# Kernel optimization log

Measured on AMD Instinct MI355X. Metric: run time of the kernel, lower is better.

The kernel has to match this reference:

```python
import jax, jax.numpy as jnp
import numpy as np

BATCH = 32768
INPUT_DIM = 256
N_NEURONS = 128
MAX_DEGREE = 7  # D; features per input dim = D+1 = 8


def _cheb_features(x, degree):
    """Chebyshev T_0..T_degree of x [B, In] -> [B, In, degree+1] via recurrence.

    Matches torch.special.chebyshev_polynomial_t(x, n=d) for d = 0..degree.
    """
    T = [jnp.ones_like(x), x]
    for _ in range(2, degree + 1):
        T.append(2.0 * x * T[-1] - T[-2])
    return jnp.stack(T[: degree + 1], axis=-1)


def setup_inputs() -> dict:
    key = jax.random.key(0)
    k1, k2 = jax.random.split(key)
    # inputs in [0,1) keep Chebyshev values bounded, as in a normalized pipeline
    x = jax.random.uniform(k1, (BATCH, INPUT_DIM), dtype=jnp.float32)
    # per-neuron coefficient vectors over the dim-major [In*(D+1)] feature layout
    coeffs = jax.random.normal(k2, (N_NEURONS, INPUT_DIM * (MAX_DEGREE + 1)), dtype=jnp.float32) * 0.02
    return {"x": x, "coeffs": coeffs}


def reference(x, coeffs):
    B, In = x.shape
    D = coeffs.shape[1] // In - 1
    # [B, In, D+1] -> dim-major flatten matches torch.cat over per-dim stacks
    X = _cheb_features(x, D).reshape(B, In * (D + 1))
    # per-neuron dot products, then sum over neurons (KANLayer stack().sum(0))
    per_neuron = jnp.einsum("bf,nf->bn", X, coeffs)  # [B, n_neurons]
    return per_neuron.sum(axis=1, keepdims=True)  # [B, 1]
```

## Files before the change

### kernel.cpp

```cpp
#include <hip/hip_runtime.h>

#define BATCH     32768
#define IN_DIM    256
#define N_NEURONS 128
#define DEG1      8
#define FEAT      (IN_DIM * DEG1)
#define F4        (FEAT / 4)
#define XR4       (IN_DIM / 4)
#define RPW       16


__global__ __launch_bounds__(256) void reduce_coeffs(const float* __restrict__ coeffs,
                                                     float* __restrict__ csum) {
    __shared__ float4 part[256];
    const int t = threadIdx.x;
    const int c = t & 7;
    const int g = t >> 3;
    const int col4 = blockIdx.x * 8 + c;

    const float4* p = (const float4*)coeffs + (size_t)(g * 4) * F4 + col4;
    float4 s = make_float4(0.f, 0.f, 0.f, 0.f);
#pragma unroll
    for (int n = 0; n < 4; ++n) {
        float4 v = p[(size_t)n * F4];
        s.x += v.x; s.y += v.y; s.z += v.z; s.w += v.w;
    }
    part[t] = s;
    __syncthreads();
#pragma unroll
    for (int stride = 128; stride >= 8; stride >>= 1) {
        if (t < stride) {
            float4 o = part[t + stride];
            float4 m = part[t];
            m.x += o.x; m.y += o.y; m.z += o.z; m.w += o.w;
            part[t] = m;
        }
        __syncthreads();
    }
    if (t < 8) ((float4*)csum)[blockIdx.x * 8 + t] = part[t];
}

__global__ __launch_bounds__(256) void kan_fwd(const float* __restrict__ x,
                                               const float* __restrict__ csum,
                                               float* __restrict__ out) {
    const int lane = threadIdx.x & 63;
    const int wave = threadIdx.x >> 6;
    const int row0 = (blockIdx.x * 4 + wave) * RPW;

    float c[4][8];
    const float4* c4 = (const float4*)csum + (size_t)lane * 8;
#pragma unroll
    for (int j = 0; j < 4; ++j) {
        float4 a = c4[j * 2];
        float4 b = c4[j * 2 + 1];
        c[j][0] = a.x; c[j][1] = a.y; c[j][2] = a.z; c[j][3] = a.w;
        c[j][4] = b.x; c[j][5] = b.y; c[j][6] = b.z; c[j][7] = b.w;
    }

    float acc[RPW];
    const float4* xr = (const float4*)x + (size_t)row0 * XR4 + lane;
#pragma unroll
    for (int r = 0; r < RPW; ++r) {
        float4 xv = xr[(size_t)r * XR4];
        float xs[4] = {xv.x, xv.y, xv.z, xv.w};
        float a = 0.f;
#pragma unroll
        for (int j = 0; j < 4; ++j) {
            const float xx = xs[j];
            const float two_x = xx + xx;
            a = fmaf(c[j][1], xx, a + c[j][0]);
            float tp = 1.f, tc = xx;
#pragma unroll
            for (int d = 2; d < 8; ++d) {
                float tn = fmaf(two_x, tc, -tp);
                a = fmaf(c[j][d], tn, a);
                tp = tc; tc = tn;
            }
        }
        acc[r] = a;
    }

#pragma unroll
    for (int rq = 0; rq < RPW / 4; ++rq) {
        float s[4];
#pragma unroll
        for (int k = 0; k < 4; ++k) {
            float a = acc[rq * 4 + k];
#pragma unroll
            for (int off = 32; off > 0; off >>= 1) a += __shfl_down(a, off, 64);
            s[k] = a;
        }
        if (lane == 0)
            ((float4*)out)[row0 / 4 + rq] = make_float4(s[0], s[1], s[2], s[3]);
    }
}

extern "C" void kernel_launch(void* const* d_in, const int* in_sizes, int n_in,
                              void* d_out, int out_size, void* d_ws, size_t ws_size,
                              hipStream_t stream) {
    const float* x      = (const float*)d_in[0];
    const float* coeffs = (const float*)d_in[1];
    float* out  = (float*)d_out;
    float* csum = (float*)d_ws;

    reduce_coeffs<<<64, 256, 0, stream>>>(coeffs, csum);
    kan_fwd<<<BATCH / (4 * RPW), 256, 0, stream>>>(x, csum, out);
}
```

Before: 77.71 us.

## Fuse coefficient reduction into main kernel with per-block shared-memory csum

Merges the coefficient-sum kernel into the forward kernel so that each of 256 large blocks reduces all 128 neuron coefficient rows into shared memory before evaluating Chebyshev terms. Input rows are prefetched into registers ahead of the reduction so their load latency overlaps it. This removes a launch and the workspace round trip, but every block redundantly reads the full coefficient matrix. It also uses fewer, larger blocks with fewer rows per wave.

Measured after the change: 193.0 us. +148.4%, slower.

```diff
diff --git a/kernel.cpp b/kernel.cpp
--- a/kernel.cpp
+++ b/kernel.cpp
@@ -5,47 +5,49 @@
 #define N_NEURONS 128
 #define DEG1      8
 #define FEAT      (IN_DIM * DEG1)
-#define F4        (FEAT / 4)
 #define XR4       (IN_DIM / 4)
-#define RPW       16
+#define NBLK      256
+#define NTHR      1024
+#define RPW       8
 
 
-__global__ __launch_bounds__(256) void reduce_coeffs(const float* __restrict__ coeffs,
-                                                     float* __restrict__ csum) {
-    __shared__ float4 part[256];
-    const int t = threadIdx.x;
-    const int c = t & 7;
-    const int g = t >> 3;
-    const int col4 = blockIdx.x * 8 + c;
+__global__ __launch_bounds__(NTHR) void kan_fused(const float* __restrict__ x,
+                                                  const float* __restrict__ coeffs,
+                                                  float* __restrict__ out) {
+    __shared__ float csum[FEAT];
+    const int t    = threadIdx.x;
+    const int lane = t & 63;
+    const int wave = t >> 6;
+    const int row0 = (blockIdx.x * (NTHR / 64) + wave) * RPW;
 
-    const float4* p = (const float4*)coeffs + (size_t)(g * 4) * F4 + col4;
-    float4 s = make_float4(0.f, 0.f, 0.f, 0.f);
+    float4 xv[RPW];
+    const float4* xr = (const float4*)x + (size_t)row0 * XR4 + lane;
 #pragma unroll
-    for (int n = 0; n < 4; ++n) {
-        float4 v = p[(size_t)n * F4];
-        s.x += v.x; s.y += v.y; s.z += v.z; s.w += v.w;
+    for (int r = 0; r < RPW; ++r) xv[r] = xr[(size_t)r * XR4];
+
+#pragma unroll
+    for (int half = 0; half < 2; ++half) {
+        const int col = t + half * NTHR;
+        float gs[32];
+#pragma unroll
+        for (int g = 0; g < 32; ++g) {
+            const float* p = coeffs + (size_t)(g * 4) * FEAT + col;
+            float s = p[0];
+            s += p[(size_t)1 * FEAT];
+            s += p[(size_t)2 * FEAT];
+            s += p[(size_t)3 * FEAT];
+            gs[g] = s;
+        }
+#pragma unroll
+        for (int stride = 16; stride >= 1; stride >>= 1) {
+#pragma unroll
+            for (int g = 0; g < 16; ++g) {
+                if (g < stride) gs[g] += gs[g + stride];
+            }
+        }
+        csum[col] = gs[0];
     }
-    part[t] = s;
     __syncthreads();
-#pragma unroll
-    for (int stride = 128; stride >= 8; stride >>= 1) {
-        if (t < stride) {
-            float4 o = part[t + stride];
-            float4 m = part[t];
-            m.x += o.x; m.y += o.y; m.z += o.z; m.w += o.w;
-            part[t] = m;
-        }
-        __syncthreads();
-    }
-    if (t < 8) ((float4*)csum)[blockIdx.x * 8 + t] = part[t];
-}
-
-__global__ __launch_bounds__(256) void kan_fwd(const float* __restrict__ x,
-                                               const float* __restrict__ csum,
-                                               float* __restrict__ out) {
-    const int lane = threadIdx.x & 63;
-    const int wave = threadIdx.x >> 6;
-    const int row0 = (blockIdx.x * 4 + wave) * RPW;
 
     float c[4][8];
     const float4* c4 = (const float4*)csum + (size_t)lane * 8;
@@ -58,11 +60,9 @@
     }
 
     float acc[RPW];
-    const float4* xr = (const float4*)x + (size_t)row0 * XR4 + lane;
 #pragma unroll
     for (int r = 0; r < RPW; ++r) {
-        float4 xv = xr[(size_t)r * XR4];
-        float xs[4] = {xv.x, xv.y, xv.z, xv.w};
+        float xs[4] = {xv[r].x, xv[r].y, xv[r].z, xv[r].w};
         float a = 0.f;
 #pragma unroll
         for (int j = 0; j < 4; ++j) {
@@ -100,9 +100,8 @@
                               hipStream_t stream) {
     const float* x      = (const float*)d_in[0];
     const float* coeffs = (const float*)d_in[1];
-    float* out  = (float*)d_out;
-    float* csum = (float*)d_ws;
+    float* out = (float*)d_out;
+    (void)d_ws; (void)ws_size;
 
-    reduce_coeffs<<<64, 256, 0, stream>>>(coeffs, csum);
-    kan_fwd<<<BATCH / (4 * RPW), 256, 0, stream>>>(x, csum, out);
+    kan_fused<<<NBLK, NTHR, 0, stream>>>(x, coeffs, out);
 }
```
